# Kernel tuning notes

Measured on AMD Instinct MI355X. Metric: run time of the kernel, lower is better.

The kernel has to match this reference:

```python
import jax, jax.numpy as jnp
import numpy as np

IN_SIZE = 1024
OUT_SIZE = 3 * IN_SIZE  # must equal 3*in_size for trigger_a * attn broadcast
B, S = 32, 512


def setup_inputs() -> dict:
    key = jax.random.key(0)
    ks = jax.random.split(key, 8)
    h_state = jax.random.normal(ks[0], (B, S, 2 * IN_SIZE), dtype=jnp.float32)
    x = jax.random.normal(ks[1], (B, S, IN_SIZE), dtype=jnp.float32)
    trigger = jax.random.randint(ks[2], (B,), 0, S)
    mask = jax.random.randint(ks[3], (B, S), 0, 2).astype(jnp.int32)
    # learned params (nn.Linear: y = x @ W.T + b; store pre-transposed as (in, out))
    Wa = jax.random.normal(ks[4], (3 * IN_SIZE, OUT_SIZE), dtype=jnp.float32) / np.sqrt(3 * IN_SIZE)
    ba = jnp.zeros((OUT_SIZE,), dtype=jnp.float32)
    Ws = jax.random.normal(ks[5], (2 * IN_SIZE, OUT_SIZE), dtype=jnp.float32) / np.sqrt(2 * IN_SIZE)
    bs = jnp.zeros((OUT_SIZE,), dtype=jnp.float32)
    return {"h_state": h_state, "x": x, "trigger": trigger, "mask": mask,
            "Wa": Wa, "ba": ba, "Ws": Ws, "bs": bs}


def reference(h_state, x, trigger, mask, Wa, ba, Ws, bs):
    # a: (B, S, 3*in_size)
    a = jnp.concatenate([h_state, x], axis=-1)
    b = a.shape[0]
    # one_hot + masked_select in the original == gather of the trigger row per batch
    trigger_a = a[jnp.arange(b), trigger]  # (B, 3*in_size)
    s = h_state.sum(axis=1)  # (B, 2*in_size)
    # et: (B, S, out_size)
    et = jnp.tanh(a @ Wa + ba + (s @ Ws + bs)[:, None, :])
    # masked_fill where mask == 0 (mask broadcast over feature dim)
    et = jnp.where(mask[:, :, None] == 0, jnp.float32(-1e9), et)
    # softmax over the FEATURE dim (dim=-1), as in the original; dropout in eval mode is identity
    attn = jax.nn.softmax(et, axis=-1)
    # trigger-weighted reduction over the sequence dim
    out = (trigger_a[:, None, :] * attn).sum(axis=1)  # (B, out_size)
    return out
```

## Files before the change

kernel.cpp:

```cpp
#include <hip/hip_runtime.h>
#include <hip/hip_bf16.h>
#include <hip/hip_fp16.h>


namespace {
constexpr int SIN  = 1024;
constexpr int KH   = 2048;
constexpr int NF   = 3072;
constexpr int NBAT = 32;
constexpr int NS   = 512;
constexpr int NM   = NBAT * NS;
constexpr int NDB  = NF / 64;
constexpr int KC   = 8;
constexpr int NKT  = NF / 64;
constexpr int NCH  = 8;
}

typedef unsigned short u16;
typedef __bf16 bf16x8 __attribute__((ext_vector_type(8)));
typedef float  f32x4  __attribute__((ext_vector_type(4)));

#define ASYNC_CP16(gptr, lptr)                                                              \
  __builtin_amdgcn_global_load_lds((__attribute__((address_space(1))) void*)(gptr),         \
                                   (__attribute__((address_space(3))) void*)(lptr), 16, 0, 0)

__device__ __forceinline__ u16 f2b(float f) {
  union { float f; unsigned u; } v; v.f = f;
  unsigned u = v.u;
  u += 0x7FFFu + ((u >> 16) & 1u);
  return (u16)(u >> 16);
}

__global__ __launch_bounds__(256) void k_prep(const int* __restrict__ mask,
                                              int* __restrict__ bcnt,
                                              int* __restrict__ boff,
                                              int* __restrict__ meta) {
  int tid = threadIdx.x;
  int b = tid >> 3, seg = tid & 7;
  int c = 0;
#pragma unroll
  for (int i = 0; i < 64; ++i) c += mask[b * NS + seg * 64 + i];
  c += __shfl_xor(c, 1, 64);
  c += __shfl_xor(c, 2, 64);
  c += __shfl_xor(c, 4, 64);
  __shared__ int sc[NBAT];
  if (seg == 0) { sc[b] = c; bcnt[b] = c; }
  __syncthreads();
  if (tid == 0) {
    int run = 0;
    for (int bb = 0; bb < NBAT; ++bb) { boff[bb] = run; run += sc[bb]; }
    meta[0] = run;
    meta[1] = (run + 255) & ~255;
  }
}

__global__ __launch_bounds__(512) void k_gather(const int* __restrict__ mask,
                                                const int* __restrict__ boff,
                                                const int* __restrict__ meta,
                                                int* __restrict__ rowmap) {
  __shared__ int ps[NS];
  int b = blockIdx.x, t = threadIdx.x;
  int m = mask[b * NS + t];
  ps[t] = m;
  __syncthreads();
#pragma unroll
  for (int off = 1; off < NS; off <<= 1) {
    int v = (t >= off) ? ps[t - off] : 0;
    __syncthreads();
    ps[t] += v;
    __syncthreads();
  }
  if (m) rowmap[boff[b] + ps[t] - m] = b * NS + t;
  if (b == 0) {
    int Mc = meta[0], McPad = meta[1];
    if (Mc + t < McPad) rowmap[Mc + t] = 0;
  }
}

__global__ __launch_bounds__(256) void k_sum_h(const float* __restrict__ h,
                                               float* __restrict__ s) {
  int b = blockIdx.x;
  int d = blockIdx.y * 256 + threadIdx.x;
  const float* p = h + (size_t)b * NS * KH + d;
  float acc = 0.f;
#pragma unroll 8
  for (int t = 0; t < NS; ++t) acc += p[(size_t)t * KH];
  s[b * KH + d] = acc;
}

__global__ __launch_bounds__(256) void k_base1(const float* __restrict__ s,
                                               const float* __restrict__ Ws,
                                               float* __restrict__ basep) {
  __shared__ float sT[NBAT][KH / KC];
  int f  = blockIdx.x * 256 + threadIdx.x;
  int k0 = blockIdx.y * (KH / KC);
  for (int it = 0; it < NBAT; ++it) {
    int idx = it * 256 + threadIdx.x;
    int b = idx >> 8, kk = idx & 255;
    sT[b][kk] = s[b * KH + k0 + kk];
  }
  __syncthreads();
  float acc[NBAT] = {};
  for (int k = 0; k < KH / KC; ++k) {
    float w = Ws[(size_t)(k0 + k) * NF + f];
#pragma unroll
    for (int b = 0; b < NBAT; ++b) acc[b] += sT[b][k] * w;
  }
#pragma unroll
  for (int b = 0; b < NBAT; ++b)
    basep[((size_t)blockIdx.y * NBAT + b) * NF + f] = acc[b];
}

__global__ __launch_bounds__(256) void k_base2(const float* __restrict__ basep,
                                               const float* __restrict__ ba,
                                               const float* __restrict__ bs,
                                               float* __restrict__ base) {
  int b = blockIdx.x;
  int f = blockIdx.y * 256 + threadIdx.x;
  float acc = 0.f;
#pragma unroll
  for (int kc = 0; kc < KC; ++kc) acc += basep[((size_t)kc * NBAT + b) * NF + f];
  base[b * NF + f] = acc + ba[f] + bs[f];
}

__global__ __launch_bounds__(256) void k_cvt_a(const float* __restrict__ h,
                                               const float* __restrict__ x,
                                               const int* __restrict__ rowmap,
                                               const int* __restrict__ meta,
                                               u16* __restrict__ A) {
  const int total = meta[1] * (NF / 4);
  for (int idx = blockIdx.x * 256 + threadIdx.x; idx < total;
       idx += gridDim.x * 256) {
    int i = idx / (NF / 4);
    int k = (idx - i * (NF / 4)) * 4;
    ushort4 o;
    if (i >= meta[0]) {
      o.x = o.y = o.z = o.w = 0;
    } else {
      int ro = rowmap[i];
      int b = ro >> 9, t = ro & 511;
      const float* src = (k < KH) ? h + ((size_t)b * NS + t) * KH + k
                                  : x + ((size_t)b * NS + t) * SIN + (k - KH);
      float4 v = *(const float4*)src;
      o.x = f2b(v.x); o.y = f2b(v.y); o.z = f2b(v.z); o.w = f2b(v.w);
    }
    *(ushort4*)(A + (size_t)i * NF + k) = o;
  }
}

__global__ __launch_bounds__(256) void k_wat(const float* __restrict__ Wa,
                                             u16* __restrict__ WaT) {
  __shared__ float tile[64][65];
  int k0 = blockIdx.x * 64, f0 = blockIdx.y * 64;
  int tid = threadIdx.x;
  int col4 = (tid & 15) * 4, row = tid >> 4;
#pragma unroll
  for (int rr = 0; rr < 64; rr += 16) {
    float4 v = *(const float4*)(Wa + (size_t)(k0 + row + rr) * NF + f0 + col4);
    tile[row + rr][col4 + 0] = v.x; tile[row + rr][col4 + 1] = v.y;
    tile[row + rr][col4 + 2] = v.z; tile[row + rr][col4 + 3] = v.w;
  }
  __syncthreads();
#pragma unroll
  for (int rr = 0; rr < 64; rr += 16) {
    int f = f0 + row + rr;
    ushort4 o;
    o.x = f2b(tile[col4 + 0][row + rr]); o.y = f2b(tile[col4 + 1][row + rr]);
    o.z = f2b(tile[col4 + 2][row + rr]); o.w = f2b(tile[col4 + 3][row + rr]);
    *(ushort4*)(WaT + (size_t)f * NF + k0 + col4) = o;
  }
}

#define LDSOFF(row, gg) ((row) * 32 + ((((gg) ^ (((row) >> 1) & 3))) << 3))

#define LDB4(BUF, KS)                                                        \
  _Pragma("unroll") for (int nf = 0; nf < 4; ++nf) {                         \
    int rb = wc * 64 + nf * 16 + lr;                                         \
    bfr[nf] = *(const bf16x8*)&lds[BUF][1][KS][LDSOFF(rb, g)];               \
  }

#define LDA4(BUF, KS, MH)                                                    \
  _Pragma("unroll") for (int mf = 0; mf < 4; ++mf) {                         \
    int ra = wr * 128 + ((MH) * 4 + mf) * 16 + lr;                           \
    afr[mf] = *(const bf16x8*)&lds[BUF][0][KS][LDSOFF(ra, g)];               \
  }

#define MFMA16(MH)                                                           \
  _Pragma("unroll") for (int mf = 0; mf < 4; ++mf)                           \
  _Pragma("unroll") for (int nf = 0; nf < 4; ++nf)                           \
    acc[(MH) * 4 + mf][nf] = __builtin_amdgcn_mfma_f32_16x16x32_bf16(        \
        afr[mf], bfr[nf], acc[(MH) * 4 + mf][nf], 0, 0, 0);

#define STAGE(SMAT, SBUF, SKS, SKT)                                          \
  if ((SKT) < NKT) {                                                         \
    _Pragma("unroll") for (int q = 0; q < 2; ++q) {                          \
      const u16* src = ((SMAT) ? pB[q] : pA[q]) + (SKT) * 64 + (SKS) * 32;   \
      ASYNC_CP16(src, &lds[SBUF][SMAT][SKS][q * 4096 + wid * 512]);          \
    }                                                                        \
  }

#define PH(BUF, KS, MH, SMAT, SBUF, SKS, SKT)                                \
  {                                                                          \
    if ((MH) == 0) { LDB4(BUF, KS) }                                         \
    LDA4(BUF, KS, MH)                                                        \
    STAGE(SMAT, SBUF, SKS, SKT)                                              \
    __builtin_amdgcn_s_setprio(1);                                           \
    MFMA16(MH)                                                               \
    __builtin_amdgcn_s_setprio(0);                                           \
    asm volatile("s_waitcnt vmcnt(6)" ::: "memory");                         \
    __builtin_amdgcn_s_barrier();                                            \
  }

__global__ __launch_bounds__(512, 2) void k_gemm(const u16* __restrict__ A,
                                                 const u16* __restrict__ Wt,
                                                 const float* __restrict__ base,
                                                 const int* __restrict__ rowmap,
                                                 const int* __restrict__ meta,
                                                 __half* __restrict__ P,
                                                 float* __restrict__ Dpart) {
  __shared__ __align__(16) u16 lds[2][2][2][8192];
  const int MT   = meta[1] >> 8;
  const int nact = MT * 12;
  const int flat = blockIdx.x;
  if (flat >= nact) return;
  const int qx = nact >> 3, rx = nact & 7;
  const int xcd = flat & 7, idx = flat >> 3;
  const int swz = (xcd < rx) ? xcd * (qx + 1) + idx
                             : rx * (qx + 1) + (xcd - rx) * qx + idx;
  const int mt = swz / 12, nt = swz - mt * 12;
  const int r0 = mt << 8, c0 = nt << 8;

  const int tid = threadIdx.x;
  const int wid = tid >> 6, lane = tid & 63;
  const int wr = wid >> 2, wc = wid & 3;
  const int g = lane >> 4, lr = lane & 15;

  const u16* pA[2]; const u16* pB[2];
#pragma unroll
  for (int q = 0; q < 2; ++q) {
    int c = q * 512 + tid;
    int row = c >> 2;
    int kc8 = (((c & 3) ^ ((row >> 1) & 3)) << 3);
    pA[q] = A  + (size_t)(r0 + row) * NF + kc8;
    pB[q] = Wt + (size_t)(c0 + row) * NF + kc8;
  }

  f32x4 acc[8][4] = {};
  bf16x8 afr[4], bfr[4];

  STAGE(0, 0, 0, 0) STAGE(1, 0, 0, 0)
  STAGE(0, 0, 1, 0) STAGE(1, 0, 1, 0)
  STAGE(0, 1, 0, 1) STAGE(1, 1, 0, 1)
  asm volatile("s_waitcnt vmcnt(8)" ::: "memory");
  __builtin_amdgcn_s_barrier();

#pragma unroll 1
  for (int i = 0; i < NKT / 2; ++i) {
    const int kt1 = 2 * i + 1, kt2 = 2 * i + 2, kt3 = 2 * i + 3;
    PH(0, 0, 0, 0, 1, 1, kt1)
    PH(0, 0, 1, 1, 1, 1, kt1)
    PH(0, 1, 0, 0, 0, 0, kt2)
    PH(0, 1, 1, 1, 0, 0, kt2)
    PH(1, 0, 0, 0, 0, 1, kt2)
    PH(1, 0, 1, 1, 0, 1, kt2)
    PH(1, 1, 0, 0, 1, 0, kt3)
    PH(1, 1, 1, 1, 1, 0, kt3)
  }

  const int cbase = c0 + wc * 64;
#pragma unroll
  for (int mf = 0; mf < 8; ++mf) {
#pragma unroll
    for (int j = 0; j < 4; ++j) {
      int i = r0 + wr * 128 + mf * 16 + g * 4 + j;
      int b = rowmap[i] >> 9;
      float rs = 0.f;
#pragma unroll
      for (int nf = 0; nf < 4; ++nf) {
        int ccn = cbase + nf * 16 + lr;
        float z  = acc[mf][nf][j] + base[b * NF + ccn];
        z        = fminf(fmaxf(z, -15.f), 15.f);
        float e2 = __expf(2.f * z);
        float th = (e2 - 1.f) / (e2 + 1.f);
        float p  = __expf(th);
        P[(size_t)i * NF + ccn] = __float2half(p);
        rs += p;
      }
#pragma unroll
      for (int off = 1; off < 16; off <<= 1) rs += __shfl_xor(rs, off, 64);
      if (lr == 0) Dpart[(size_t)i * NDB + (cbase >> 6)] = rs;
    }
  }
}

__global__ __launch_bounds__(256) void k_invd(const float* __restrict__ Dpart,
                                              const int* __restrict__ meta,
                                              float* __restrict__ invD) {
  int i = blockIdx.x * 256 + threadIdx.x;
  if (i >= meta[1]) return;
  float d = 0.f;
#pragma unroll
  for (int q = 0; q < NDB; ++q) d += Dpart[(size_t)i * NDB + q];
  invD[i] = 1.0f / d;
}

__global__ __launch_bounds__(256) void k_final1(const __half* __restrict__ P,
                                                const float* __restrict__ invD,
                                                const int* __restrict__ boff,
                                                const int* __restrict__ bcnt,
                                                float* __restrict__ pb) {
  int c = blockIdx.x;
  int b = c >> 3, j = c & 7;
  int f = blockIdx.y * 512 + threadIdx.x * 2;
  int cnt = bcnt[b];
  int lo = j * 64, hi = min(cnt, lo + 64);
  int off = boff[b];
  __shared__ float ivs[64];
  if (threadIdx.x < 64 && lo + (int)threadIdx.x < hi)
    ivs[threadIdx.x] = invD[off + lo + threadIdx.x];
  __syncthreads();
  float ax = 0.f, ay = 0.f;
  for (int t = lo; t < hi; ++t) {
    __half2 hv = *(const __half2*)(P + (size_t)(off + t) * NF + f);
    float2 fv = __half22float2(hv);
    float iv = ivs[t - lo];
    ax += fv.x * iv; ay += fv.y * iv;
  }
  float2 o; o.x = ax; o.y = ay;
  *(float2*)(pb + (size_t)c * NF + f) = o;
}

__global__ __launch_bounds__(256) void k_final2(const float* __restrict__ pb,
                                                const int* __restrict__ bcnt,
                                                const float* __restrict__ h,
                                                const float* __restrict__ x,
                                                const int* __restrict__ trig,
                                                float* __restrict__ out) {
  int b = blockIdx.x;
  int f = blockIdx.y * 256 + threadIdx.x;
  float acc = 0.f;
#pragma unroll
  for (int j = 0; j < NCH; ++j) acc += pb[(size_t)(b * NCH + j) * NF + f];
  acc += (float)(NS - bcnt[b]) * (1.0f / (float)NF);
  int tr = trig[b];
  float ta = (f < KH) ? h[((size_t)b * NS + tr) * KH + f]
                      : x[((size_t)b * NS + tr) * SIN + f - KH];
  out[b * NF + f] = acc * ta;
}

extern "C" void kernel_launch(void* const* d_in, const int* in_sizes, int n_in,
                              void* d_out, int out_size, void* d_ws, size_t ws_size,
                              hipStream_t stream) {
  const float* h_state = (const float*)d_in[0];
  const float* x       = (const float*)d_in[1];
  const int*   trigger = (const int*)d_in[2];
  const int*   mask    = (const int*)d_in[3];
  const float* Wa      = (const float*)d_in[4];
  const float* ba      = (const float*)d_in[5];
  const float* Ws      = (const float*)d_in[6];
  const float* bs      = (const float*)d_in[7];
  float*       out     = (float*)d_out;

  char* w = (char*)d_ws;
  u16*    Abf   = (u16*)w;                 w += (size_t)NM * NF * 2;
  u16*    WaT   = (u16*)w;                 w += (size_t)NF * NF * 2;
  __half* P     = (__half*)w;              w += (size_t)NM * NF * 2;
  float*  s     = (float*)w;               w += (size_t)NBAT * KH * 4;
  float*  base  = (float*)w;               w += (size_t)NBAT * NF * 4;
  float*  Dpart = (float*)w;               w += (size_t)NM * NDB * 4;
  float*  basep = (float*)Dpart;
  float*  pb    = (float*)Dpart;
  float*  invD  = (float*)w;               w += (size_t)NM * 4;
  int*    rowmap= (int*)w;                 w += (size_t)NM * 4;
  int*    bcnt  = (int*)w;                 w += 128;
  int*    boff  = (int*)w;                 w += 128;
  int*    meta  = (int*)w;                 w += 128;

  (void)in_sizes; (void)n_in; (void)out_size; (void)ws_size;

  k_prep  <<<dim3(1), 256, 0, stream>>>(mask, bcnt, boff, meta);
  k_gather<<<dim3(NBAT), 512, 0, stream>>>(mask, boff, meta, rowmap);
  k_sum_h <<<dim3(NBAT, KH / 256), 256, 0, stream>>>(h_state, s);
  k_cvt_a <<<dim3(2048), 256, 0, stream>>>(h_state, x, rowmap, meta, Abf);
  k_wat   <<<dim3(NF / 64, NF / 64), 256, 0, stream>>>(Wa, WaT);
  k_base1 <<<dim3(NF / 256, KC), 256, 0, stream>>>(s, Ws, basep);
  k_base2 <<<dim3(NBAT, NF / 256), 256, 0, stream>>>(basep, ba, bs, base);
  k_gemm  <<<dim3((NF / 256) * (NM / 256)), 512, 0, stream>>>(Abf, WaT, base, rowmap, meta, P, Dpart);
  k_invd  <<<dim3(NM / 256), 256, 0, stream>>>(Dpart, meta, invD);
  k_final1<<<dim3(NBAT * NCH, NF / 512), 256, 0, stream>>>(P, invD, boff, bcnt, pb);
  k_final2<<<dim3(NBAT, NF / 256), 256, 0, stream>>>(pb, bcnt, h_state, x, trigger, out);
}
```

Baseline: 399.0 us.

## Fuse h-sum with bf16 gather conversion and relax GEMM waitcnt barriers

Merges the sequence-sum of h_state and the compacted bf16 conversion of A into a single kernel, so h_state is read once instead of twice. A per-row rank array scatters converted rows, and padding-row zeroing moves into k_gather. The GEMM now waits on vmcnt only twice per iteration instead of every phase, and k_base1 processes four k values per step with float4 shared-memory reads. The fused kernel uses only 384 blocks that each walk 512 rows serially and issue 2-byte scattered stores, and the looser waitcnt may be too weak if the prefetch depth is miscounted.

```diff
diff --git a/kernel.cpp b/kernel.cpp
--- a/kernel.cpp
+++ b/kernel.cpp
@@ -57,7 +57,9 @@
 __global__ __launch_bounds__(512) void k_gather(const int* __restrict__ mask,
                                                 const int* __restrict__ boff,
                                                 const int* __restrict__ meta,
-                                                int* __restrict__ rowmap) {
+                                                int* __restrict__ rowmap,
+                                                int* __restrict__ rank,
+                                                u16* __restrict__ A) {
   __shared__ int ps[NS];
   int b = blockIdx.x, t = threadIdx.x;
   int m = mask[b * NS + t];
@@ -70,22 +72,53 @@
     ps[t] += v;
     __syncthreads();
   }
-  if (m) rowmap[boff[b] + ps[t] - m] = b * NS + t;
-  if (b == 0) {
-    int Mc = meta[0], McPad = meta[1];
-    if (Mc + t < McPad) rowmap[Mc + t] = 0;
-  }
-}
-
-__global__ __launch_bounds__(256) void k_sum_h(const float* __restrict__ h,
-                                               float* __restrict__ s) {
-  int b = blockIdx.x;
-  int d = blockIdx.y * 256 + threadIdx.x;
-  const float* p = h + (size_t)b * NS * KH + d;
-  float acc = 0.f;
-#pragma unroll 8
-  for (int t = 0; t < NS; ++t) acc += p[(size_t)t * KH];
-  s[b * KH + d] = acc;
+  if (m) {
+    int idx = boff[b] + ps[t] - 1;
+    rowmap[idx] = b * NS + t;
+    rank[b * NS + t] = idx;
+  }
+  int Mc = meta[0], pad = meta[1] - Mc;
+  if (b == 0 && t < 256) { if (t < pad) rowmap[Mc + t] = 0; }
+  for (int r = b; r < pad; r += NBAT) {
+    unsigned* row = (unsigned*)(A + (size_t)(Mc + r) * NF);
+    for (int u = t; u < NF / 2; u += 512) row[u] = 0;
+  }
+}
+
+__global__ __launch_bounds__(256) void k_sumcvt(const float* __restrict__ h,
+                                                const float* __restrict__ x,
+                                                const int* __restrict__ mask,
+                                                const int* __restrict__ rank,
+                                                float* __restrict__ s,
+                                                u16* __restrict__ A) {
+  int b = blockIdx.x, cb = blockIdx.y, tid = threadIdx.x;
+  __shared__ int ms[NS];
+  __shared__ int rk[NS];
+  for (int u = tid; u < NS; u += 256) {
+    int m = mask[b * NS + u];
+    ms[u] = m;
+    rk[u] = m ? rank[b * NS + u] : 0;
+  }
+  __syncthreads();
+  if (cb < 8) {
+    int d = cb * 256 + tid;
+    const float* hb = h + (size_t)b * NS * KH + d;
+    float acc = 0.f;
+#pragma unroll 4
+    for (int t = 0; t < NS; ++t) {
+      float v = hb[(size_t)t * KH];
+      acc += v;
+      if (ms[t]) A[(size_t)rk[t] * NF + d] = f2b(v);
+    }
+    s[b * KH + d] = acc;
+  } else {
+    int d = (cb - 8) * 256 + tid;
+    const float* xb = x + (size_t)b * NS * SIN + d;
+#pragma unroll 4
+    for (int t = 0; t < NS; ++t) {
+      if (ms[t]) A[(size_t)rk[t] * NF + KH + d] = f2b(xb[(size_t)t * SIN]);
+    }
+  }
 }
 
 __global__ __launch_bounds__(256) void k_base1(const float* __restrict__ s,
@@ -101,10 +134,16 @@
   }
   __syncthreads();
   float acc[NBAT] = {};
-  for (int k = 0; k < KH / KC; ++k) {
-    float w = Ws[(size_t)(k0 + k) * NF + f];
-#pragma unroll
-    for (int b = 0; b < NBAT; ++b) acc[b] += sT[b][k] * w;
+  for (int k = 0; k < KH / KC; k += 4) {
+    float w0 = Ws[(size_t)(k0 + k + 0) * NF + f];
+    float w1 = Ws[(size_t)(k0 + k + 1) * NF + f];
+    float w2 = Ws[(size_t)(k0 + k + 2) * NF + f];
+    float w3 = Ws[(size_t)(k0 + k + 3) * NF + f];
+#pragma unroll
+    for (int b = 0; b < NBAT; ++b) {
+      float4 sv = *(const float4*)&sT[b][k];
+      acc[b] += sv.x * w0 + sv.y * w1 + sv.z * w2 + sv.w * w3;
+    }
   }
 #pragma unroll
   for (int b = 0; b < NBAT; ++b)
@@ -123,31 +162,6 @@
   base[b * NF + f] = acc + ba[f] + bs[f];
 }
 
-__global__ __launch_bounds__(256) void k_cvt_a(const float* __restrict__ h,
-                                               const float* __restrict__ x,
-                                               const int* __restrict__ rowmap,
-                                               const int* __restrict__ meta,
-                                               u16* __restrict__ A) {
-  const int total = meta[1] * (NF / 4);
-  for (int idx = blockIdx.x * 256 + threadIdx.x; idx < total;
-       idx += gridDim.x * 256) {
-    int i = idx / (NF / 4);
-    int k = (idx - i * (NF / 4)) * 4;
-    ushort4 o;
-    if (i >= meta[0]) {
-      o.x = o.y = o.z = o.w = 0;
-    } else {
-      int ro = rowmap[i];
-      int b = ro >> 9, t = ro & 511;
-      const float* src = (k < KH) ? h + ((size_t)b * NS + t) * KH + k
-                                  : x + ((size_t)b * NS + t) * SIN + (k - KH);
-      float4 v = *(const float4*)src;
-      o.x = f2b(v.x); o.y = f2b(v.y); o.z = f2b(v.z); o.w = f2b(v.w);
-    }
-    *(ushort4*)(A + (size_t)i * NF + k) = o;
-  }
-}
-
 __global__ __launch_bounds__(256) void k_wat(const float* __restrict__ Wa,
                                              u16* __restrict__ WaT) {
   __shared__ float tile[64][65];
@@ -199,7 +213,7 @@
     }                                                                        \
   }
 
-#define PH(BUF, KS, MH, SMAT, SBUF, SKS, SKT)                                \
+#define PH(BUF, KS, MH, SMAT, SBUF, SKS, SKT, VM)                            \
   {                                                                          \
     if ((MH) == 0) { LDB4(BUF, KS) }                                         \
     LDA4(BUF, KS, MH)                                                        \
@@ -207,7 +221,7 @@
     __builtin_amdgcn_s_setprio(1);                                           \
     MFMA16(MH)                                                               \
     __builtin_amdgcn_s_setprio(0);                                           \
-    asm volatile("s_waitcnt vmcnt(6)" ::: "memory");                         \
+    if (VM) asm volatile("s_waitcnt vmcnt(4)" ::: "memory");                 \
     __builtin_amdgcn_s_barrier();                                            \
   }
 
@@ -251,20 +265,20 @@
   STAGE(0, 0, 0, 0) STAGE(1, 0, 0, 0)
   STAGE(0, 0, 1, 0) STAGE(1, 0, 1, 0)
   STAGE(0, 1, 0, 1) STAGE(1, 1, 0, 1)
-  asm volatile("s_waitcnt vmcnt(8)" ::: "memory");
+  asm volatile("s_waitcnt vmcnt(4)" ::: "memory");
   __builtin_amdgcn_s_barrier();
 
 #pragma unroll 1
   for (int i = 0; i < NKT / 2; ++i) {
     const int kt1 = 2 * i + 1, kt2 = 2 * i + 2, kt3 = 2 * i + 3;
-    PH(0, 0, 0, 0, 1, 1, kt1)
-    PH(0, 0, 1, 1, 1, 1, kt1)
-    PH(0, 1, 0, 0, 0, 0, kt2)
-    PH(0, 1, 1, 1, 0, 0, kt2)
-    PH(1, 0, 0, 0, 0, 1, kt2)
-    PH(1, 0, 1, 1, 0, 1, kt2)
-    PH(1, 1, 0, 0, 1, 0, kt3)
-    PH(1, 1, 1, 1, 1, 0, kt3)
+    PH(0, 0, 0, 0, 1, 1, kt1, 0)
+    PH(0, 0, 1, 1, 1, 1, kt1, 0)
+    PH(0, 1, 0, 0, 0, 0, kt2, 0)
+    PH(0, 1, 1, 1, 0, 0, kt2, 1)
+    PH(1, 0, 0, 0, 0, 1, kt2, 0)
+    PH(1, 0, 1, 1, 0, 1, kt2, 0)
+    PH(1, 1, 0, 0, 1, 0, kt3, 0)
+    PH(1, 1, 1, 1, 1, 0, kt3, 1)
   }
 
   const int cbase = c0 + wc * 64;
@@ -372,6 +386,7 @@
   float*  pb    = (float*)Dpart;
   float*  invD  = (float*)w;               w += (size_t)NM * 4;
   int*    rowmap= (int*)w;                 w += (size_t)NM * 4;
+  int*    rank  = (int*)w;                 w += (size_t)NM * 4;
   int*    bcnt  = (int*)w;                 w += 128;
   int*    boff  = (int*)w;                 w += 128;
   int*    meta  = (int*)w;                 w += 128;
@@ -379,9 +394,8 @@
   (void)in_sizes; (void)n_in; (void)out_size; (void)ws_size;
 
   k_prep  <<<dim3(1), 256, 0, stream>>>(mask, bcnt, boff, meta);
-  k_gather<<<dim3(NBAT), 512, 0, stream>>>(mask, boff, meta, rowmap);
-  k_sum_h <<<dim3(NBAT, KH / 256), 256, 0, stream>>>(h_state, s);
-  k_cvt_a <<<dim3(2048), 256, 0, stream>>>(h_state, x, rowmap, meta, Abf);
+  k_gather<<<dim3(NBAT), 512, 0, stream>>>(mask, boff, meta, rowmap, rank, Abf);
+  k_sumcvt<<<dim3(NBAT, 12), 256, 0, stream>>>(h_state, x, mask, rank, s, Abf);
   k_wat   <<<dim3(NF / 64, NF / 64), 256, 0, stream>>>(Wa, WaT);
   k_base1 <<<dim3(NF / 256, KC), 256, 0, stream>>>(s, Ws, basep);
   k_base2 <<<dim3(NBAT, NF / 256), 256, 0, stream>>>(basep, ba, bs, base);
```

New measurement: 504.0 us. +26.3%, slower.
